# Kernel optimization log

Measured on AMD Instinct MI355X. Metric: run time of the kernel, lower is better.

Reference implementation:

```python
import jax, jax.numpy as jnp
import numpy as np

EPS = 1e-8
SIGMA_MIN = 1e-4
B, T, C, P = 32, 8192, 64, 168


def setup_inputs() -> dict:
    key = jax.random.key(0)
    k1, k2, k3, k4, k5 = jax.random.split(key, 5)
    x_full = jax.random.normal(k1, (B, T, C), dtype=jnp.float32)
    mask = (jax.random.uniform(k2, (B, T, C)) > 0.2).astype(jnp.float32)
    x = mask * x_full  # observed input with missing positions zeroed
    phase_id = jax.random.randint(k3, (B,), 0, P, dtype=jnp.int64)
    anchor_mu = jax.random.normal(k4, (P, C), dtype=jnp.float32)
    anchor_log_sigma = 0.1 * jax.random.normal(k5, (P, C), dtype=jnp.float32)
    return {
        "x": x,
        "mask": mask,
        "phase_id": phase_id,
        "anchor_mu": anchor_mu,
        "anchor_log_sigma": anchor_log_sigma,
        "tau0_raw": jnp.zeros((1,), dtype=jnp.float32),
        "tau1_raw": jnp.zeros((1,), dtype=jnp.float32),
        "missing_token": jnp.zeros((1, 1, C), dtype=jnp.float32),
    }


def _max_gap_ratio(mask):
    # longest contiguous missing run (channel 0) as fraction of T -> (B,1,1)
    missing = mask[:, :, 0] < 0.5  # (B, T)
    Tlen = missing.shape[1]
    idx = jnp.arange(Tlen)[None, :]  # (1, T)
    # index of most recent observed position (running max), -1 if none yet
    last_obs = jax.lax.associative_scan(jnp.maximum,
                                        jnp.where(missing, -1, idx), axis=1)
    run = jnp.where(missing, idx - last_obs, 0)  # current missing run length
    max_run = run.max(axis=1).astype(jnp.float32)
    return (max_run / Tlen)[:, None, None]


def reference(x, mask, phase_id, anchor_mu, anchor_log_sigma,
              tau0_raw, tau1_raw, missing_token):
    # masked moments over time axis
    mask_sum = jnp.clip(mask.sum(axis=1, keepdims=True), EPS, None)  # (B,1,C)
    mu_obs = (mask * x).sum(axis=1, keepdims=True) / mask_sum
    var_obs = (mask * (x - mu_obs) ** 2).sum(axis=1, keepdims=True) / mask_sum
    sigma_obs = jnp.sqrt(var_obs + EPS)

    # anchor lookup
    mu_ref = anchor_mu[phase_id][:, None, :]              # (B,1,C)
    log_sigma_ref = anchor_log_sigma[phase_id][:, None, :]

    coverage = mask.mean(axis=1, keepdims=True)           # (B,1,C)
    gap_ratio = _max_gap_ratio(mask)                      # (B,1,1)

    tau0 = jax.nn.softplus(tau0_raw)
    tau1 = jax.nn.softplus(tau1_raw)
    w = coverage / (coverage + tau0 + tau1 * gap_ratio + EPS)

    mu = w * mu_obs + (1.0 - w) * mu_ref
    log_sigma = w * jnp.log(sigma_obs + EPS) + (1.0 - w) * log_sigma_ref
    sigma = jnp.clip(jnp.exp(log_sigma), SIGMA_MIN, None)

    z = (x - mu) / sigma
    return mask * z + (1.0 - mask) * missing_token
```

## Files before the change

### kernel.cpp

```cpp
#include <hip/hip_runtime.h>
#include <math.h>

#define B_ 32
#define T_ 8192
#define C_ 64
#define S_ 256
#define L_ 32
#define EPS_ 1e-8f
#define SIGMA_MIN_ 1e-4f

#define SUM_OFF 0
#define SQ_OFF  524288
#define MS_OFF  1048576
#define GAP_OFF 1572864
#define MU_OFF  1605632
#define INV_OFF 1607680

__device__ inline float4 f4add(float4 a, float4 b) {
    return make_float4(a.x + b.x, a.y + b.y, a.z + b.z, a.w + b.w);
}
__device__ inline float4 f4shfl_xor(float4 v, int m) {
    float4 r;
    r.x = __shfl_xor(v.x, m);
    r.y = __shfl_xor(v.y, m);
    r.z = __shfl_xor(v.z, m);
    r.w = __shfl_xor(v.w, m);
    return r;
}
__device__ inline void merge_lr(int l_pre, int l_suf, int l_best, int l_len,
                                int r_pre, int r_suf, int r_best, int r_len,
                                int& pre, int& suf, int& best, int& len) {
    best = max(max(l_best, r_best), l_suf + r_pre);
    pre  = (l_pre == l_len) ? l_len + r_pre : l_pre;
    suf  = (r_suf == r_len) ? r_len + l_suf : r_suf;
    len  = l_len + r_len;
}

__global__ __launch_bounds__(512) void k1_stats(const float* __restrict__ x,
                                                const float* __restrict__ mask,
                                                float* __restrict__ ws) {
    const int bid = blockIdx.x;
    const int b   = bid >> 8;
    const int s   = bid & (S_ - 1);
    const int tid = threadIdx.x;
    const int cq  = tid & 15;
    const int tr  = tid >> 4;
    const int wv  = tid >> 6;

    const long gi = ((long)b * T_ + (long)s * L_ + tr) * 16 + cq;
    const float4 xv = ((const float4*)x)[gi];
    const float4 mv = ((const float4*)mask)[gi];

    __shared__ unsigned char misbyte[L_];
    if (cq == 0) misbyte[tr] = (mv.x < 0.5f) ? 1 : 0;

    float4 s1 = xv;
    float4 s2 = make_float4(xv.x * xv.x, xv.y * xv.y, xv.z * xv.z, xv.w * xv.w);
    float4 sm = mv;

    s1 = f4add(s1, f4shfl_xor(s1, 16)); s1 = f4add(s1, f4shfl_xor(s1, 32));
    s2 = f4add(s2, f4shfl_xor(s2, 16)); s2 = f4add(s2, f4shfl_xor(s2, 32));
    sm = f4add(sm, f4shfl_xor(sm, 16)); sm = f4add(sm, f4shfl_xor(sm, 32));

    __shared__ float4 shA[8][16];
    __shared__ float4 shB[8][16];
    __shared__ float4 shC[8][16];
    if ((tid & 63) < 16) { shA[wv][cq] = s1; shB[wv][cq] = s2; shC[wv][cq] = sm; }
    __syncthreads();

    if (tid < 16) {
        float4 a = f4add(f4add(f4add(shA[0][tid], shA[1][tid]), f4add(shA[2][tid], shA[3][tid])),
                         f4add(f4add(shA[4][tid], shA[5][tid]), f4add(shA[6][tid], shA[7][tid])));
        float4 c = f4add(f4add(f4add(shB[0][tid], shB[1][tid]), f4add(shB[2][tid], shB[3][tid])),
                         f4add(f4add(shB[4][tid], shB[5][tid]), f4add(shB[6][tid], shB[7][tid])));
        float4 e = f4add(f4add(f4add(shC[0][tid], shC[1][tid]), f4add(shC[2][tid], shC[3][tid])),
                         f4add(f4add(shC[4][tid], shC[5][tid]), f4add(shC[6][tid], shC[7][tid])));
        ((float4*)(ws + SUM_OFF))[bid * 16 + tid] = a;
        ((float4*)(ws + SQ_OFF ))[bid * 16 + tid] = c;
        ((float4*)(ws + MS_OFF ))[bid * 16 + tid] = e;
    }

    if (tid < 32) {
        const int miss = misbyte[tid];
        unsigned long long bal = __ballot(miss != 0);
        if (tid == 0) {
            unsigned int w = (unsigned int)bal;
            int pre, suf, best;
            if (w == 0xFFFFFFFFu) {
                pre = 32; suf = 32; best = 32;
            } else {
                pre = __builtin_ctz(~w);
                suf = __builtin_clz(~w);
                unsigned int tmp = w; best = 0;
                while (tmp) { tmp &= (tmp << 1); ++best; }
            }
            ((int4*)((int*)(ws + GAP_OFF)))[bid] = make_int4(pre, suf, best, L_);
        }
    }
}

__global__ __launch_bounds__(256) void k2_params(const int*   __restrict__ phase_id,
                                                 const float* __restrict__ anchor_mu,
                                                 const float* __restrict__ anchor_ls,
                                                 const float* __restrict__ tau0_raw,
                                                 const float* __restrict__ tau1_raw,
                                                 float* __restrict__ ws) {
    const int b   = blockIdx.x;
    const int tid = threadIdx.x;
    const int q   = tid & 15;
    const int p   = tid >> 4;

    float4 a1 = make_float4(0.f, 0.f, 0.f, 0.f);
    float4 a2 = make_float4(0.f, 0.f, 0.f, 0.f);
    float4 am = make_float4(0.f, 0.f, 0.f, 0.f);
#pragma unroll
    for (int i = 0; i < 16; ++i) {
        const int idx = (b * S_ + (p + i * 16)) * 16 + q;
        a1 = f4add(a1, ((const float4*)(ws + SUM_OFF))[idx]);
        a2 = f4add(a2, ((const float4*)(ws + SQ_OFF ))[idx]);
        am = f4add(am, ((const float4*)(ws + MS_OFF ))[idx]);
    }

    __shared__ float shf[3][16][64];
    *(float4*)&shf[0][p][q * 4] = a1;
    *(float4*)&shf[1][p][q * 4] = a2;
    *(float4*)&shf[2][p][q * 4] = am;
    __syncthreads();

    if (tid < 64) {
        const int4* gp = (const int4*)((const int*)(ws + GAP_OFF)) + b * S_;
        int pre, suf, best, len;
        {
            int4 t0 = gp[tid * 4];
            pre = t0.x; suf = t0.y; best = t0.z; len = t0.w;
        }
#pragma unroll
        for (int k = 1; k < 4; ++k) {
            int4 r = gp[tid * 4 + k];
            merge_lr(pre, suf, best, len, r.x, r.y, r.z, r.w, pre, suf, best, len);
        }
#pragma unroll
        for (int m = 1; m < 64; m <<= 1) {
            int ppre = __shfl_xor(pre, m);
            int psuf = __shfl_xor(suf, m);
            int pbest = __shfl_xor(best, m);
            int plen = __shfl_xor(len, m);
            if (tid & m)
                merge_lr(ppre, psuf, pbest, plen, pre, suf, best, len,
                         pre, suf, best, len);
            else
                merge_lr(pre, suf, best, len, ppre, psuf, pbest, plen,
                         pre, suf, best, len);
        }
        const float gap = (float)best / (float)T_;

        const int c = tid;
        float sum = 0.f, sq = 0.f, ms = 0.f;
#pragma unroll
        for (int pp = 0; pp < 16; ++pp) {
            sum += shf[0][pp][c];
            sq  += shf[1][pp][c];
            ms  += shf[2][pp][c];
        }

        const float msc    = fmaxf(ms, EPS_);
        const float mu_obs = sum / msc;
        float var = (sq - 2.f * mu_obs * sum + mu_obs * mu_obs * ms) / msc;
        var = fmaxf(var, 0.f);
        const float sigma_obs = sqrtf(var + EPS_);
        const float coverage  = ms / (float)T_;

        const float t0 = log1pf(expf(tau0_raw[0]));
        const float t1 = log1pf(expf(tau1_raw[0]));
        const float w  = coverage / (coverage + t0 + t1 * gap + EPS_);

        const int   pid    = phase_id[b];
        const float mu_ref = anchor_mu[pid * C_ + c];
        const float ls_ref = anchor_ls[pid * C_ + c];

        const float mu = w * mu_obs + (1.f - w) * mu_ref;
        const float ls = w * logf(sigma_obs + EPS_) + (1.f - w) * ls_ref;
        const float sigma = fmaxf(expf(ls), SIGMA_MIN_);

        ws[MU_OFF  + b * C_ + c] = mu;
        ws[INV_OFF + b * C_ + c] = 1.f / sigma;
    }
}

__global__ __launch_bounds__(256) void k3_norm(const float* __restrict__ x,
                                               const float* __restrict__ mask,
                                               const float* __restrict__ token,
                                               const float* __restrict__ ws,
                                               float* __restrict__ out) {
    const int gid = blockIdx.x * 256 + threadIdx.x;
    const float4* x4 = (const float4*)x;
    const float4* m4 = (const float4*)mask;
    const float4* mu4  = (const float4*)(ws + MU_OFF);
    const float4* inv4 = (const float4*)(ws + INV_OFF);
    const float4* tk4  = (const float4*)token;

    const int b = gid >> 17;
    const int p = b * 16 + (gid & 15);

    float4 xv = x4[gid];
    float4 mv = m4[gid];
    float4 mu = mu4[p];
    float4 iv = inv4[p];
    float4 tk = tk4[gid & 15];

    float4 o;
    o.x = mv.x * ((xv.x - mu.x) * iv.x) + (1.f - mv.x) * tk.x;
    o.y = mv.y * ((xv.y - mu.y) * iv.y) + (1.f - mv.y) * tk.y;
    o.z = mv.z * ((xv.z - mu.z) * iv.z) + (1.f - mv.z) * tk.z;
    o.w = mv.w * ((xv.w - mu.w) * iv.w) + (1.f - mv.w) * tk.w;

    ((float4*)out)[gid] = o;
}

extern "C" void kernel_launch(void* const* d_in, const int* in_sizes, int n_in,
                              void* d_out, int out_size, void* d_ws, size_t ws_size,
                              hipStream_t stream) {
    const float* x    = (const float*)d_in[0];
    const float* mask = (const float*)d_in[1];
    const int*   pid  = (const int*)  d_in[2];
    const float* amu  = (const float*)d_in[3];
    const float* als  = (const float*)d_in[4];
    const float* t0   = (const float*)d_in[5];
    const float* t1   = (const float*)d_in[6];
    const float* tok  = (const float*)d_in[7];
    float* out = (float*)d_out;
    float* ws  = (float*)d_ws;

    k1_stats<<<B_ * S_, 512, 0, stream>>>(x, mask, ws);
    k2_params<<<B_, 256, 0, stream>>>(pid, amu, als, t0, t1, ws);
    const int n4 = B_ * T_ * C_ / 4;
    k3_norm<<<n4 / 256, 256, 0, stream>>>(x, mask, tok, ws, out);
}
```

Before: 64.37 us.

## Pack mask into ballot bitmasks in stats pass and drop mask reread

The stats kernel now ballots the mask per wavefront and writes four 64-bit bitmasks per wave to workspace. The normalize kernel reads these bitmasks instead of the full float mask, so it loads far less mask data, and it selects between the normalized value and the token instead of blending them. It also writes the output with nontemporal stores. The cost is extra small writes in the first kernel, and the select assumes the mask is binary (0/1), which the task guarantees.

```diff
diff --git a/kernel.cpp b/kernel.cpp
--- a/kernel.cpp
+++ b/kernel.cpp
@@ -9,12 +9,18 @@
 #define EPS_ 1e-8f
 #define SIGMA_MIN_ 1e-4f
 
-#define SUM_OFF 0
-#define SQ_OFF  524288
-#define MS_OFF  1048576
-#define GAP_OFF 1572864
-#define MU_OFF  1605632
-#define INV_OFF 1607680
+typedef float vfloat4 __attribute__((ext_vector_type(4)));
+
+#define SUM_OFF  0
+#define SQ_OFF   524288
+#define MS_OFF   1048576
+#define GAP_OFF  1572864
+#define BITX_OFF 1605632
+#define BITY_OFF 1736704
+#define BITZ_OFF 1867776
+#define BITW_OFF 1998848
+#define MU_OFF   2129920
+#define INV_OFF  2131968
 
 __device__ inline float4 f4add(float4 a, float4 b) {
     return make_float4(a.x + b.x, a.y + b.y, a.z + b.z, a.w + b.w);
@@ -50,6 +56,18 @@
     const long gi = ((long)b * T_ + (long)s * L_ + tr) * 16 + cq;
     const float4 xv = ((const float4*)x)[gi];
     const float4 mv = ((const float4*)mask)[gi];
+
+    unsigned long long balx = __ballot(mv.x >= 0.5f);
+    unsigned long long baly = __ballot(mv.y >= 0.5f);
+    unsigned long long balz = __ballot(mv.z >= 0.5f);
+    unsigned long long balw = __ballot(mv.w >= 0.5f);
+    if ((tid & 63) == 0) {
+        const int wi = bid * 8 + wv;
+        ((unsigned long long*)(ws + BITX_OFF))[wi] = balx;
+        ((unsigned long long*)(ws + BITY_OFF))[wi] = baly;
+        ((unsigned long long*)(ws + BITZ_OFF))[wi] = balz;
+        ((unsigned long long*)(ws + BITW_OFF))[wi] = balw;
+    }
 
     __shared__ unsigned char misbyte[L_];
     if (cq == 0) misbyte[tr] = (mv.x < 0.5f) ? 1 : 0;
@@ -188,13 +206,11 @@
 }
 
 __global__ __launch_bounds__(256) void k3_norm(const float* __restrict__ x,
-                                               const float* __restrict__ mask,
                                                const float* __restrict__ token,
                                                const float* __restrict__ ws,
                                                float* __restrict__ out) {
     const int gid = blockIdx.x * 256 + threadIdx.x;
     const float4* x4 = (const float4*)x;
-    const float4* m4 = (const float4*)mask;
     const float4* mu4  = (const float4*)(ws + MU_OFF);
     const float4* inv4 = (const float4*)(ws + INV_OFF);
     const float4* tk4  = (const float4*)token;
@@ -202,19 +218,25 @@
     const int b = gid >> 17;
     const int p = b * 16 + (gid & 15);
 
+    const int wi = gid >> 6;
+    const int ln = gid & 63;
+    const unsigned long long wx = ((const unsigned long long*)(ws + BITX_OFF))[wi];
+    const unsigned long long wy = ((const unsigned long long*)(ws + BITY_OFF))[wi];
+    const unsigned long long wz = ((const unsigned long long*)(ws + BITZ_OFF))[wi];
+    const unsigned long long wwd = ((const unsigned long long*)(ws + BITW_OFF))[wi];
+
     float4 xv = x4[gid];
-    float4 mv = m4[gid];
     float4 mu = mu4[p];
     float4 iv = inv4[p];
     float4 tk = tk4[gid & 15];
 
-    float4 o;
-    o.x = mv.x * ((xv.x - mu.x) * iv.x) + (1.f - mv.x) * tk.x;
-    o.y = mv.y * ((xv.y - mu.y) * iv.y) + (1.f - mv.y) * tk.y;
-    o.z = mv.z * ((xv.z - mu.z) * iv.z) + (1.f - mv.z) * tk.z;
-    o.w = mv.w * ((xv.w - mu.w) * iv.w) + (1.f - mv.w) * tk.w;
-
-    ((float4*)out)[gid] = o;
+    vfloat4 o;
+    o.x = ((wx  >> ln) & 1) ? (xv.x - mu.x) * iv.x : tk.x;
+    o.y = ((wy  >> ln) & 1) ? (xv.y - mu.y) * iv.y : tk.y;
+    o.z = ((wz  >> ln) & 1) ? (xv.z - mu.z) * iv.z : tk.z;
+    o.w = ((wwd >> ln) & 1) ? (xv.w - mu.w) * iv.w : tk.w;
+
+    __builtin_nontemporal_store(o, (vfloat4*)out + gid);
 }
 
 extern "C" void kernel_launch(void* const* d_in, const int* in_sizes, int n_in,
@@ -234,5 +256,5 @@
     k1_stats<<<B_ * S_, 512, 0, stream>>>(x, mask, ws);
     k2_params<<<B_, 256, 0, stream>>>(pid, amu, als, t0, t1, ws);
     const int n4 = B_ * T_ * C_ / 4;
-    k3_norm<<<n4 / 256, 256, 0, stream>>>(x, mask, tok, ws, out);
-}
+    k3_norm<<<n4 / 256, 256, 0, stream>>>(x, tok, ws, out);
+}
```

New measurement: 67.44 us. 1.05x slower.
